# Optimization experiments

Hardware: AMD Instinct MI355X
Metric: run time of the kernel (lower is better)

Reference implementation:

```python
import jax, jax.numpy as jnp
import numpy as np

N_NODES = 50000
N_EDGES = 1000000
NUM_FEATURES = 32
EDGE_DIM = 16
H = 64
L = 2
BN_EPS = 1e-5
GIN_EPS = 0.0


def _lin(k, fan_in, fan_out, scale=0.1):
    kw, kb = jax.random.split(k)
    W = jax.random.normal(kw, (fan_in, fan_out), jnp.float32) * scale
    b = jax.random.normal(kb, (fan_out,), jnp.float32) * scale
    return W, b


def setup_inputs() -> dict:
    key = jax.random.key(0)
    ks = jax.random.split(key, 12)
    x = jax.random.normal(ks[0], (N_NODES, NUM_FEATURES), jnp.float32)
    edge_index = jax.random.randint(ks[1], (2, N_EDGES), 0, N_NODES, jnp.int64 if jax.config.read('jax_enable_x64') else jnp.int32)
    edge_attr = jax.random.normal(ks[2], (N_EDGES, EDGE_DIM), jnp.float32)
    node_W, node_b = _lin(ks[3], NUM_FEATURES, H)
    edge_W, edge_b = _lin(ks[4], EDGE_DIM, H)

    def stack_lin(k, fan_in, fan_out):
        Ws, bs = zip(*[_lin(kk, fan_in, fan_out) for kk in jax.random.split(k, L)])
        return jnp.stack(Ws), jnp.stack(bs)

    elin_W, elin_b = stack_lin(ks[5], H, H)      # GINEConv internal edge lin
    mlp1_W, mlp1_b = stack_lin(ks[6], H, H)      # GINEConv nn layer 1
    mlp2_W, mlp2_b = stack_lin(ks[7], H, H)      # GINEConv nn layer 2
    emlp1_W, emlp1_b = stack_lin(ks[8], 3 * H, H)  # edge-update MLP layer 1
    emlp2_W, emlp2_b = stack_lin(ks[9], H, H)      # edge-update MLP layer 2
    bn_gamma = jnp.ones((L, H), jnp.float32)
    bn_beta = jnp.zeros((L, H), jnp.float32)
    return dict(x=x, edge_index=edge_index, edge_attr=edge_attr,
                node_W=node_W, node_b=node_b, edge_W=edge_W, edge_b=edge_b,
                elin_W=elin_W, elin_b=elin_b,
                mlp1_W=mlp1_W, mlp1_b=mlp1_b, mlp2_W=mlp2_W, mlp2_b=mlp2_b,
                emlp1_W=emlp1_W, emlp1_b=emlp1_b, emlp2_W=emlp2_W, emlp2_b=emlp2_b,
                bn_gamma=bn_gamma, bn_beta=bn_beta)


def reference(x, edge_index, edge_attr,
              node_W, node_b, edge_W, edge_b,
              elin_W, elin_b, mlp1_W, mlp1_b, mlp2_W, mlp2_b,
              emlp1_W, emlp1_b, emlp2_W, emlp2_b, bn_gamma, bn_beta):
    src, dst = edge_index[0], edge_index[1]
    n = x.shape[0]
    h = x @ node_W + node_b                     # [N, H]
    ea = edge_attr @ edge_W + edge_b            # [E, H]
    for i in range(L):
        # GINEConv: message = relu(x_src + lin(edge_attr)), sum-aggregate at dst
        msg = jax.nn.relu(h[src] + ea @ elin_W[i] + elin_b[i])        # [E, H]
        agg = jax.ops.segment_sum(msg, dst, num_segments=n)           # [N, H]
        out = (1.0 + GIN_EPS) * h + agg
        out = jax.nn.relu(out @ mlp1_W[i] + mlp1_b[i]) @ mlp2_W[i] + mlp2_b[i]
        # BatchNorm (training-mode batch statistics, biased variance)
        mu = out.mean(axis=0)
        var = out.var(axis=0)
        out = (out - mu) * jax.lax.rsqrt(var + BN_EPS) * bn_gamma[i] + bn_beta[i]
        h = (h + jax.nn.relu(out)) * 0.5
        # edge update: gather-concat-MLP residual
        e_in = jnp.concatenate([h[src], h[dst], ea], axis=-1)         # [E, 3H]
        e_up = jax.nn.relu(e_in @ emlp1_W[i] + emlp1_b[i]) @ emlp2_W[i] + emlp2_b[i]
        ea = ea + e_up * 0.5
    return h, ea
```

## Files before the change

kernel.cpp:

```cpp
#include <hip/hip_runtime.h>
#include <hip/hip_bf16.h>

#define NN 50000
#define NE 1000000
#define NF 32
#define ED 16
#define HD 64
#define BN_EPS 1e-5f

typedef unsigned short u16;
typedef __attribute__((ext_vector_type(8))) short bf16x8;
typedef __attribute__((ext_vector_type(4))) float f32x4;

#define WAVE_SYNC() do { \
    asm volatile("s_waitcnt lgkmcnt(0)" ::: "memory"); \
    __builtin_amdgcn_sched_barrier(0); \
} while (0)

__device__ __forceinline__ u16 f2b(float x)
{
    __hip_bfloat16 b = __float2bfloat16(x);
    u16 u; __builtin_memcpy(&u, &b, 2); return u;
}
__device__ __forceinline__ float b2f(u16 u)
{
    uint v = (uint)u << 16; float f; __builtin_memcpy(&f, &v, 4); return f;
}

__global__ __launch_bounds__(256) void k_fill(float* p, float v, size_t n)
{
    size_t i = (size_t)blockIdx.x * 256 + threadIdx.x;
    if (i < n) p[i] = v;
}

__device__ __forceinline__ void gemm4(float (&o)[HD], float4 t, const float* __restrict__ Wr)
{
    #pragma unroll
    for (int f = 0; f < HD; f++) o[f] = fmaf(t.x, Wr[f], o[f]);
    #pragma unroll
    for (int f = 0; f < HD; f++) o[f] = fmaf(t.y, Wr[HD + f], o[f]);
    #pragma unroll
    for (int f = 0; f < HD; f++) o[f] = fmaf(t.z, Wr[2 * HD + f], o[f]);
    #pragma unroll
    for (int f = 0; f < HD; f++) o[f] = fmaf(t.w, Wr[3 * HD + f], o[f]);
}

__device__ __forceinline__ bf16x8 pack8(const float* __restrict__ p)
{
    float4 v0 = ((const float4*)p)[0];
    float4 v1 = ((const float4*)p)[1];
    union { uint u[4]; bf16x8 v; } r;
    r.u[0] = (uint)f2b(v0.x) | ((uint)f2b(v0.y) << 16);
    r.u[1] = (uint)f2b(v0.z) | ((uint)f2b(v0.w) << 16);
    r.u[2] = (uint)f2b(v1.x) | ((uint)f2b(v1.y) << 16);
    r.u[3] = (uint)f2b(v1.z) | ((uint)f2b(v1.w) << 16);
    return r.v;
}

__global__ __launch_bounds__(256) void k_prep_all(
    const float* __restrict__ W1, const float* __restrict__ W2,
    const float* __restrict__ We, const float* __restrict__ Wp,
    u16* __restrict__ w1t, u16* __restrict__ w2t,
    u16* __restrict__ welt, u16* __restrict__ wpad)
{
    int idx = blockIdx.x * 256 + threadIdx.x;
    if (idx < 24576) {
        int l = idx / (192 * HD), r = idx % (192 * HD), k = r / HD, f = r % HD;
        w1t[l * 192 * HD + f * 192 + k] = f2b(W1[idx]);
    } else if (idx < 32768) {
        int i = idx - 24576;
        int l = i / (HD * HD), r = i % (HD * HD), k = r / HD, f = r % HD;
        w2t[l * HD * HD + f * HD + k] = f2b(W2[i]);
    } else if (idx < 40960) {
        int i = idx - 32768;
        int l = i / (HD * HD), r = i % (HD * HD), k = r / HD, f = r % HD;
        welt[l * HD * HD + f * HD + k] = f2b(We[i]);
    } else if (idx < 43008) {
        int i = idx - 40960;
        int f = i / 32, k = i % 32;
        wpad[f * 32 + k] = (k < ED) ? f2b(Wp[k * HD + f]) : (u16)0;
    }
}

__global__ __launch_bounds__(256) void k_node_proj(
    const float* __restrict__ x, const float* __restrict__ W,
    const float* __restrict__ b, float* __restrict__ h, float* __restrict__ agg)
{
    __shared__ float sW[NF * HD];
    for (int t = threadIdx.x; t < NF * HD; t += 256) sW[t] = W[t];
    __syncthreads();
    int lane = threadIdx.x & 63, wv = threadIdx.x >> 6;
    int n = blockIdx.x * 4 + wv;
    if (n >= NN) return;
    float a = (lane < NF) ? x[(size_t)n * NF + lane] : 0.f;
    float acc = b[lane];
    #pragma unroll
    for (int k = 0; k < NF; k++) acc = fmaf(__shfl(a, k), sW[k * HD + lane], acc);
    h[(size_t)n * HD + lane] = acc;
    agg[(size_t)n * HD + lane] = 0.f;
}

__global__ __launch_bounds__(256) void k_edge_proj_gine(
    const float* __restrict__ attr, const float* __restrict__ h,
    const int* __restrict__ src, const int* __restrict__ dst,
    const u16* __restrict__ wpadt, const float* __restrict__ eb,
    const u16* __restrict__ welt, const float* __restrict__ belin,
    u16* __restrict__ eab, float* __restrict__ agg, float* __restrict__ bnst)
{
    __shared__ u16 sO[4][32 * 72];
    const int lane = threadIdx.x & 63, wv = threadIdx.x >> 6;
    if (blockIdx.x == 0 && threadIdx.x < 128) bnst[threadIdx.x] = 0.f;
    const size_t base = ((size_t)blockIdx.x * 4 + wv) * 32;
    if (base >= NE) return;
    u16* sOw = sO[wv];
    const int c = lane & 15, g = lane >> 4;

    bf16x8 zero8 = {0, 0, 0, 0, 0, 0, 0, 0};
    bf16x8 ap[2];
    #pragma unroll
    for (int s = 0; s < 2; s++)
        ap[s] = (g < 2) ? pack8(attr + (base + 16 * s + c) * ED + 8 * g) : zero8;

    f32x4 acc[2][4];
    #pragma unroll
    for (int s = 0; s < 2; s++)
        #pragma unroll
        for (int tt = 0; tt < 4; tt++) {
            float bv = eb[tt * 16 + c];
            acc[s][tt] = (f32x4){bv, bv, bv, bv};
        }
    #pragma unroll
    for (int tt = 0; tt < 4; tt++) {
        bf16x8 bw = *(const bf16x8*)&wpadt[(tt * 16 + c) * 32 + 8 * g];
        acc[0][tt] = __builtin_amdgcn_mfma_f32_16x16x32_bf16(ap[0], bw, acc[0][tt], 0, 0, 0);
        acc[1][tt] = __builtin_amdgcn_mfma_f32_16x16x32_bf16(ap[1], bw, acc[1][tt], 0, 0, 0);
    }
    #pragma unroll
    for (int s = 0; s < 2; s++)
        #pragma unroll
        for (int tt = 0; tt < 4; tt++)
            #pragma unroll
            for (int r = 0; r < 4; r++) {
                u16 nb = f2b(acc[s][tt][r]);
                eab[(base + 16 * s + 4 * g + r) * HD + tt * 16 + c] = nb;
                sOw[(16 * s + 4 * g + r) * 72 + tt * 16 + c] = nb;
            }
    WAVE_SYNC();

    bf16x8 A3[2][2];
    #pragma unroll
    for (int s = 0; s < 2; s++) {
        A3[s][0] = *(const bf16x8*)&sOw[(16 * s + c) * 72 + 8 * g];
        A3[s][1] = *(const bf16x8*)&sOw[(16 * s + c) * 72 + 32 + 8 * g];
    }
    f32x4 acc3[2][4];
    #pragma unroll
    for (int s = 0; s < 2; s++)
        #pragma unroll
        for (int tt = 0; tt < 4; tt++) {
            float bv = belin[tt * 16 + c];
            acc3[s][tt] = (f32x4){bv, bv, bv, bv};
        }
    #pragma unroll
    for (int ki = 0; ki < 2; ki++)
        #pragma unroll
        for (int tt = 0; tt < 4; tt++) {
            bf16x8 bw = *(const bf16x8*)&welt[(tt * 16 + c) * HD + ki * 32 + 8 * g];
            acc3[0][tt] = __builtin_amdgcn_mfma_f32_16x16x32_bf16(A3[0][ki], bw, acc3[0][tt], 0, 0, 0);
            acc3[1][tt] = __builtin_amdgcn_mfma_f32_16x16x32_bf16(A3[1][ki], bw, acc3[1][tt], 0, 0, 0);
        }
    int sv2[2][4], dv2[2][4];
    #pragma unroll
    for (int s = 0; s < 2; s++)
        #pragma unroll
        for (int r = 0; r < 4; r++) {
            sv2[s][r] = src[base + 16 * s + 4 * g + r];
            dv2[s][r] = dst[base + 16 * s + 4 * g + r];
        }
    #pragma unroll
    for (int s = 0; s < 2; s++)
        #pragma unroll
        for (int tt = 0; tt < 4; tt++)
            #pragma unroll
            for (int r = 0; r < 4; r++) {
                float m = fmaxf(acc3[s][tt][r] + h[(size_t)sv2[s][r] * HD + tt * 16 + c], 0.f);
                unsafeAtomicAdd(&agg[(size_t)dv2[s][r] * HD + tt * 16 + c], m);
            }
}

__global__ __launch_bounds__(256) void k_node_mlp(
    const float* __restrict__ h, const float* __restrict__ agg,
    const float* __restrict__ W1, const float* __restrict__ b1,
    const float* __restrict__ W2, const float* __restrict__ b2,
    float* __restrict__ out2)
{
    int n = blockIdx.x * 256 + threadIdx.x;
    if (n >= NN) return;
    float o[HD];
    #pragma unroll
    for (int f = 0; f < HD; f++) o[f] = b1[f];
    const float4* hr = (const float4*)(h + (size_t)n * HD);
    const float4* ar = (const float4*)(agg + (size_t)n * HD);
    #pragma unroll 4
    for (int k4 = 0; k4 < 16; k4++) {
        float4 t1 = hr[k4], t2 = ar[k4];
        float4 t = make_float4(t1.x + t2.x, t1.y + t2.y, t1.z + t2.z, t1.w + t2.w);
        gemm4(o, t, W1 + (k4 * 4) * HD);
    }
    #pragma unroll
    for (int k = 0; k < HD; k++) o[k] = fmaxf(o[k], 0.f);
    #pragma unroll
    for (int c = 0; c < 4; c++) {
        float p[16];
        #pragma unroll
        for (int j = 0; j < 16; j++) p[j] = b2[c * 16 + j];
        for (int k = 0; k < HD; k++) {
            const float* Wr = W2 + k * HD + c * 16;
            #pragma unroll
            for (int j = 0; j < 16; j++) p[j] = fmaf(o[k], Wr[j], p[j]);
        }
        float4* orow = (float4*)(out2 + (size_t)n * HD + c * 16);
        #pragma unroll
        for (int q = 0; q < 4; q++)
            orow[q] = make_float4(p[4*q], p[4*q+1], p[4*q+2], p[4*q+3]);
    }
}

__global__ __launch_bounds__(256) void k_bnstats(
    const float* __restrict__ out2, float* __restrict__ bnst)
{
    int f = threadIdx.x & 63;
    int row0 = blockIdx.x * 4 + (threadIdx.x >> 6);
    float s = 0.f, q = 0.f;
    for (int r = row0; r < NN; r += gridDim.x * 4) {
        float v = out2[(size_t)r * HD + f];
        s += v; q += v * v;
    }
    unsafeAtomicAdd(&bnst[f], s);
    unsafeAtomicAdd(&bnst[HD + f], q);
}

__global__ __launch_bounds__(256) void k_bn_h(
    const float* __restrict__ out2, const float* __restrict__ bnst,
    const float* __restrict__ gamma, const float* __restrict__ beta,
    float* __restrict__ h, u16* __restrict__ hbf, float* __restrict__ hout,
    float* __restrict__ agg, int last)
{
    size_t idx = (size_t)blockIdx.x * 256 + threadIdx.x;
    if (idx >= (size_t)NN * HD) return;
    int f = (int)(idx & 63);
    float mu  = bnst[f] * (1.f / NN);
    float var = bnst[HD + f] * (1.f / NN) - mu * mu;
    float sc  = gamma[f] * rsqrtf(var + BN_EPS);
    float sh  = beta[f] - mu * sc;
    float o   = fmaxf(fmaf(out2[idx], sc, sh), 0.f);
    float hn  = (h[idx] + o) * 0.5f;
    h[idx] = hn;
    hbf[idx] = f2b(hn);
    if (last) hout[idx] = hn;
    else      agg[idx] = 0.f;
}

__device__ __forceinline__ void edge_mlp_core(
    const u16* __restrict__ hbf, const u16* __restrict__ eab,
    const int* __restrict__ src, const int* __restrict__ dst,
    const u16* __restrict__ w1t, const float* __restrict__ b1,
    const u16* __restrict__ w2t, const float* __restrict__ b2,
    u16* sOw, size_t base, int c, int g, f32x4 (&acc2)[2][4])
{
    int sv[2], dv[2];
    #pragma unroll
    for (int s = 0; s < 2; s++) {
        sv[s] = src[base + 16 * s + c];
        dv[s] = dst[base + 16 * s + c];
    }
    bf16x8 A[3][2][2];
    #pragma unroll
    for (int s = 0; s < 2; s++) {
        const u16* hs = &hbf[(size_t)sv[s] * HD + 8 * g];
        A[0][s][0] = *(const bf16x8*)hs;
        A[0][s][1] = *(const bf16x8*)(hs + 32);
        const u16* hd = &hbf[(size_t)dv[s] * HD + 8 * g];
        A[1][s][0] = *(const bf16x8*)hd;
        A[1][s][1] = *(const bf16x8*)(hd + 32);
        const u16* ep = &eab[(base + 16 * s + c) * HD + 8 * g];
        A[2][s][0] = *(const bf16x8*)ep;
        A[2][s][1] = *(const bf16x8*)(ep + 32);
    }
    f32x4 acc[2][4];
    #pragma unroll
    for (int s = 0; s < 2; s++)
        #pragma unroll
        for (int tt = 0; tt < 4; tt++) {
            float bv = b1[tt * 16 + c];
            acc[s][tt] = (f32x4){bv, bv, bv, bv};
        }
    #pragma unroll
    for (int sec = 0; sec < 3; sec++)
        #pragma unroll
        for (int ki = 0; ki < 2; ki++)
            #pragma unroll
            for (int tt = 0; tt < 4; tt++) {
                bf16x8 bw = *(const bf16x8*)&w1t[(tt * 16 + c) * 192 + sec * 64 + ki * 32 + 8 * g];
                acc[0][tt] = __builtin_amdgcn_mfma_f32_16x16x32_bf16(A[sec][0][ki], bw, acc[0][tt], 0, 0, 0);
                acc[1][tt] = __builtin_amdgcn_mfma_f32_16x16x32_bf16(A[sec][1][ki], bw, acc[1][tt], 0, 0, 0);
            }
    #pragma unroll
    for (int s = 0; s < 2; s++)
        #pragma unroll
        for (int tt = 0; tt < 4; tt++)
            #pragma unroll
            for (int r = 0; r < 4; r++)
                sOw[(16 * s + 4 * g + r) * 72 + tt * 16 + c] = f2b(fmaxf(acc[s][tt][r], 0.f));
    WAVE_SYNC();
    bf16x8 A2[2][2];
    #pragma unroll
    for (int s = 0; s < 2; s++) {
        A2[s][0] = *(const bf16x8*)&sOw[(16 * s + c) * 72 + 8 * g];
        A2[s][1] = *(const bf16x8*)&sOw[(16 * s + c) * 72 + 32 + 8 * g];
    }
    WAVE_SYNC();
    #pragma unroll
    for (int s = 0; s < 2; s++)
        #pragma unroll
        for (int tt = 0; tt < 4; tt++) {
            float bv = b2[tt * 16 + c];
            acc2[s][tt] = (f32x4){bv, bv, bv, bv};
        }
    #pragma unroll
    for (int ki = 0; ki < 2; ki++)
        #pragma unroll
        for (int tt = 0; tt < 4; tt++) {
            bf16x8 bw = *(const bf16x8*)&w2t[(tt * 16 + c) * HD + ki * 32 + 8 * g];
            acc2[0][tt] = __builtin_amdgcn_mfma_f32_16x16x32_bf16(A2[0][ki], bw, acc2[0][tt], 0, 0, 0);
            acc2[1][tt] = __builtin_amdgcn_mfma_f32_16x16x32_bf16(A2[1][ki], bw, acc2[1][tt], 0, 0, 0);
        }
}

__global__ __launch_bounds__(256) void k_edge_upd_fused(
    const u16* __restrict__ hbf, u16* __restrict__ eab,
    const int* __restrict__ src, const int* __restrict__ dst,
    const u16* __restrict__ w1t, const float* __restrict__ b1,
    const u16* __restrict__ w2t, const float* __restrict__ b2,
    const float* __restrict__ h, const u16* __restrict__ welt,
    const float* __restrict__ belin, float* __restrict__ agg,
    float* __restrict__ bnst)
{
    __shared__ u16 sO[4][32 * 72];
    const int lane = threadIdx.x & 63, wv = threadIdx.x >> 6;
    if (blockIdx.x == 0 && threadIdx.x < 128) bnst[threadIdx.x] = 0.f;
    const size_t base = ((size_t)blockIdx.x * 4 + wv) * 32;
    if (base >= NE) return;
    u16* sOw = sO[wv];
    const int c = lane & 15, g = lane >> 4;

    f32x4 acc2[2][4];
    edge_mlp_core(hbf, eab, src, dst, w1t, b1, w2t, b2, sOw, base, c, g, acc2);

    #pragma unroll
    for (int s = 0; s < 2; s++)
        #pragma unroll
        for (int tt = 0; tt < 4; tt++)
            #pragma unroll
            for (int r = 0; r < 4; r++) {
                size_t a = (base + 16 * s + 4 * g + r) * HD + tt * 16 + c;
                u16 nb = f2b(b2f(eab[a]) + 0.5f * acc2[s][tt][r]);
                eab[a] = nb;
                sOw[(16 * s + 4 * g + r) * 72 + tt * 16 + c] = nb;
            }
    WAVE_SYNC();

    bf16x8 A3[2][2];
    #pragma unroll
    for (int s = 0; s < 2; s++) {
        A3[s][0] = *(const bf16x8*)&sOw[(16 * s + c) * 72 + 8 * g];
        A3[s][1] = *(const bf16x8*)&sOw[(16 * s + c) * 72 + 32 + 8 * g];
    }
    f32x4 acc3[2][4];
    #pragma unroll
    for (int s = 0; s < 2; s++)
        #pragma unroll
        for (int tt = 0; tt < 4; tt++) {
            float bv = belin[tt * 16 + c];
            acc3[s][tt] = (f32x4){bv, bv, bv, bv};
        }
    #pragma unroll
    for (int ki = 0; ki < 2; ki++)
        #pragma unroll
        for (int tt = 0; tt < 4; tt++) {
            bf16x8 bw = *(const bf16x8*)&welt[(tt * 16 + c) * HD + ki * 32 + 8 * g];
            acc3[0][tt] = __builtin_amdgcn_mfma_f32_16x16x32_bf16(A3[0][ki], bw, acc3[0][tt], 0, 0, 0);
            acc3[1][tt] = __builtin_amdgcn_mfma_f32_16x16x32_bf16(A3[1][ki], bw, acc3[1][tt], 0, 0, 0);
        }
    int sv2[2][4], dv2[2][4];
    #pragma unroll
    for (int s = 0; s < 2; s++)
        #pragma unroll
        for (int r = 0; r < 4; r++) {
            sv2[s][r] = src[base + 16 * s + 4 * g + r];
            dv2[s][r] = dst[base + 16 * s + 4 * g + r];
        }
    #pragma unroll
    for (int s = 0; s < 2; s++)
        #pragma unroll
        for (int tt = 0; tt < 4; tt++)
            #pragma unroll
            for (int r = 0; r < 4; r++) {
                float m = fmaxf(acc3[s][tt][r] + h[(size_t)sv2[s][r] * HD + tt * 16 + c], 0.f);
                unsafeAtomicAdd(&agg[(size_t)dv2[s][r] * HD + tt * 16 + c], m);
            }
}

__global__ __launch_bounds__(256) void k_edge_upd_final(
    const u16* __restrict__ hbf, const u16* __restrict__ eab,
    float* __restrict__ eaout,
    const int* __restrict__ src, const int* __restrict__ dst,
    const u16* __restrict__ w1t, const float* __restrict__ b1,
    const u16* __restrict__ w2t, const float* __restrict__ b2)
{
    __shared__ u16 sO[4][32 * 72];
    const int lane = threadIdx.x & 63, wv = threadIdx.x >> 6;
    const size_t base = ((size_t)blockIdx.x * 4 + wv) * 32;
    if (base >= NE) return;
    u16* sOw = sO[wv];
    const int c = lane & 15, g = lane >> 4;

    f32x4 acc2[2][4];
    edge_mlp_core(hbf, eab, src, dst, w1t, b1, w2t, b2, sOw, base, c, g, acc2);

    #pragma unroll
    for (int s = 0; s < 2; s++)
        #pragma unroll
        for (int tt = 0; tt < 4; tt++)
            #pragma unroll
            for (int r = 0; r < 4; r++) {
                size_t a = (base + 16 * s + 4 * g + r) * HD + tt * 16 + c;
                eaout[a] = b2f(eab[a]) + 0.5f * acc2[s][tt][r];
            }
}

extern "C" void kernel_launch(void* const* d_in, const int* in_sizes, int n_in,
                              void* d_out, int out_size, void* d_ws, size_t ws_size,
                              hipStream_t stream)
{
    const float* x        = (const float*)d_in[0];
    const int*   ei       = (const int*)d_in[1];
    const float* eattr    = (const float*)d_in[2];
    const float* node_W   = (const float*)d_in[3];
    const float* node_b   = (const float*)d_in[4];
    const float* edge_W   = (const float*)d_in[5];
    const float* edge_b   = (const float*)d_in[6];
    const float* elin_W   = (const float*)d_in[7];
    const float* elin_b   = (const float*)d_in[8];
    const float* mlp1_W   = (const float*)d_in[9];
    const float* mlp1_b   = (const float*)d_in[10];
    const float* mlp2_W   = (const float*)d_in[11];
    const float* mlp2_b   = (const float*)d_in[12];
    const float* emlp1_W  = (const float*)d_in[13];
    const float* emlp1_b  = (const float*)d_in[14];
    const float* emlp2_W  = (const float*)d_in[15];
    const float* emlp2_b  = (const float*)d_in[16];
    const float* bn_gamma = (const float*)d_in[17];
    const float* bn_beta  = (const float*)d_in[18];

    float* hout = (float*)d_out;
    float* eaout = hout + (size_t)NN * HD;

    const int* src = ei;
    const int* dst = ei + NE;

    float* hbuf = (float*)d_ws;
    float* agg  = hbuf + (size_t)NN * HD;
    float* out2 = agg + (size_t)NN * HD;
    float* bnst = out2 + (size_t)NN * HD;
    u16*   w1t  = (u16*)(bnst + 128);
    u16*   w2t  = w1t + 2 * 192 * HD;
    u16*   welt = w2t + 2 * HD * HD;
    u16*   wpad = welt + 2 * HD * HD;
    u16*   hbf  = wpad + HD * 32;
    u16*   eab  = hbf + (size_t)NN * HD;
    size_t base_need = ((size_t)NN * HD * 3 + 128) * sizeof(float)
                     + (2 * 192 * HD + 4 * HD * HD + HD * 32 + (size_t)NN * HD
                        + (size_t)NE * HD) * sizeof(u16);

    static const int exp_sizes[19] = {
        1600000, 2000000, 16000000, 2048, 64, 1024, 64,
        8192, 128, 8192, 128, 8192, 128, 24576, 128, 8192, 128, 128, 128};
    float sentinel = 0.f;
    if (n_in != 19) sentinel = 6000.f;
    else {
        for (int i = 0; i < 19; i++)
            if (in_sizes[i] != exp_sizes[i]) { sentinel = 2000.f + 32.f * i; break; }
    }
    if (sentinel == 0.f && ws_size < base_need) sentinel = 7000.f;
    if (sentinel != 0.f) {
        k_fill<<<dim3((unsigned)(((size_t)NN * HD + 255) / 256)), dim3(256), 0, stream>>>(
            hout, sentinel, (size_t)NN * HD);
        k_fill<<<dim3((unsigned)(((size_t)NE * HD + 255) / 256)), dim3(256), 0, stream>>>(
            eaout, 0.f, (size_t)NE * HD);
        return;
    }

    dim3 b256(256);
    const unsigned WG2 = (NE + 127) / 128;
    k_prep_all<<<dim3((43008 + 255) / 256), b256, 0, stream>>>(
        emlp1_W, emlp2_W, elin_W, edge_W, w1t, w2t, welt, wpad);
    k_node_proj<<<dim3((NN + 3) / 4), b256, 0, stream>>>(x, node_W, node_b, hbuf, agg);

    k_edge_proj_gine<<<dim3(WG2), b256, 0, stream>>>(
        eattr, hbuf, src, dst, wpad, edge_b, welt, elin_b, eab, agg, bnst);
    k_node_mlp<<<dim3((NN + 255) / 256), b256, 0, stream>>>(
        hbuf, agg, mlp1_W, mlp1_b, mlp2_W, mlp2_b, out2);
    k_bnstats<<<dim3(256), b256, 0, stream>>>(out2, bnst);
    k_bn_h<<<dim3((NN * HD + 255) / 256), b256, 0, stream>>>(
        out2, bnst, bn_gamma, bn_beta, hbuf, hbf, hout, agg, 0);
    k_edge_upd_fused<<<dim3(WG2), b256, 0, stream>>>(
        hbf, eab, src, dst, w1t, emlp1_b, w2t, emlp2_b,
        hbuf, welt + (size_t)HD * HD, elin_b + HD, agg, bnst);

    k_node_mlp<<<dim3((NN + 255) / 256), b256, 0, stream>>>(
        hbuf, agg, mlp1_W + HD * HD, mlp1_b + HD,
        mlp2_W + HD * HD, mlp2_b + HD, out2);
    k_bnstats<<<dim3(256), b256, 0, stream>>>(out2, bnst);
    k_bn_h<<<dim3((NN * HD + 255) / 256), b256, 0, stream>>>(
        out2, bnst, bn_gamma + HD, bn_beta + HD, hbuf, hbf, hout, agg, 1);
    k_edge_upd_final<<<dim3(WG2), b256, 0, stream>>>(
        hbf, eab, eaout, src, dst,
        w1t + (size_t)192 * HD, emlp1_b + HD,
        w2t + (size_t)HD * HD, emlp2_b + HD);
}
```

Baseline: 988.6 us.

## Replace atomic scatter-add aggregation with CSR gather over bf16 messages

Builds a destination-sorted CSR (histogram, single-block scan, atomic scatter of edge ids) each call. The GINE message kernels now write bf16 messages into the output buffer instead of doing float atomics into agg. A new per-node gather kernel then sums them. This removes 64M float atomics per layer and the agg zeroing, at the cost of CSR build kernels, an extra 128MB message write and read per layer, and bf16 rounding of messages before summation.

```diff
diff --git a/kernel.cpp b/kernel.cpp
--- a/kernel.cpp
+++ b/kernel.cpp
@@ -82,9 +82,68 @@
     }
 }
 
+__global__ __launch_bounds__(256) void k_hist(
+    const int* __restrict__ dst, int* __restrict__ cnt)
+{
+    for (size_t e = (size_t)blockIdx.x * 256 + threadIdx.x; e < NE;
+         e += (size_t)gridDim.x * 256)
+        atomicAdd(&cnt[dst[e]], 1);
+}
+#define SCHUNK 49
+__global__ __launch_bounds__(1024) void k_scan(
+    const int* __restrict__ cnt, int* __restrict__ rowptr, int* __restrict__ woff)
+{
+    __shared__ int ssum[1024];
+    int t = threadIdx.x;
+    int beg = t * SCHUNK, end = min(beg + SCHUNK, NN);
+    int s = 0;
+    for (int i = beg; i < end; i++) s += cnt[i];
+    ssum[t] = s;
+    __syncthreads();
+    for (int off = 1; off < 1024; off <<= 1) {
+        int v = (t >= off) ? ssum[t - off] : 0;
+        __syncthreads();
+        ssum[t] += v;
+        __syncthreads();
+    }
+    int run = (t == 0) ? 0 : ssum[t - 1];
+    for (int i = beg; i < end; i++) {
+        rowptr[i] = run; woff[i] = run;
+        run += cnt[i];
+    }
+    if (t == 1023) rowptr[NN] = run;
+}
+__global__ __launch_bounds__(256) void k_scatter(
+    const int* __restrict__ dst, int* __restrict__ woff, int* __restrict__ eidx)
+{
+    for (size_t e = (size_t)blockIdx.x * 256 + threadIdx.x; e < NE;
+         e += (size_t)gridDim.x * 256) {
+        int slot = atomicAdd(&woff[dst[e]], 1);
+        eidx[slot] = (int)e;
+    }
+}
+
+__global__ __launch_bounds__(256) void k_aggregate(
+    const u16* __restrict__ msg, const int* __restrict__ rowptr,
+    const int* __restrict__ eidx, float* __restrict__ agg)
+{
+    int lane = threadIdx.x & 63, wv = threadIdx.x >> 6;
+    int n = blockIdx.x * 4 + wv;
+    if (n >= NN) return;
+    int b = rowptr[n], e = rowptr[n + 1];
+    float s = 0.f;
+    int j = b;
+    for (; j + 1 < e; j += 2) {
+        int e0 = eidx[j], e1 = eidx[j + 1];
+        s += b2f(msg[(size_t)e0 * HD + lane]) + b2f(msg[(size_t)e1 * HD + lane]);
+    }
+    if (j < e) s += b2f(msg[(size_t)eidx[j] * HD + lane]);
+    agg[(size_t)n * HD + lane] = s;
+}
+
 __global__ __launch_bounds__(256) void k_node_proj(
     const float* __restrict__ x, const float* __restrict__ W,
-    const float* __restrict__ b, float* __restrict__ h, float* __restrict__ agg)
+    const float* __restrict__ b, float* __restrict__ h)
 {
     __shared__ float sW[NF * HD];
     for (int t = threadIdx.x; t < NF * HD; t += 256) sW[t] = W[t];
@@ -97,15 +156,14 @@
     #pragma unroll
     for (int k = 0; k < NF; k++) acc = fmaf(__shfl(a, k), sW[k * HD + lane], acc);
     h[(size_t)n * HD + lane] = acc;
-    agg[(size_t)n * HD + lane] = 0.f;
 }
 
 __global__ __launch_bounds__(256) void k_edge_proj_gine(
     const float* __restrict__ attr, const float* __restrict__ h,
-    const int* __restrict__ src, const int* __restrict__ dst,
+    const int* __restrict__ src,
     const u16* __restrict__ wpadt, const float* __restrict__ eb,
     const u16* __restrict__ welt, const float* __restrict__ belin,
-    u16* __restrict__ eab, float* __restrict__ agg, float* __restrict__ bnst)
+    u16* __restrict__ eab, u16* __restrict__ msgb, float* __restrict__ bnst)
 {
     __shared__ u16 sO[4][32 * 72];
     const int lane = threadIdx.x & 63, wv = threadIdx.x >> 6;
@@ -169,14 +227,12 @@
             acc3[0][tt] = __builtin_amdgcn_mfma_f32_16x16x32_bf16(A3[0][ki], bw, acc3[0][tt], 0, 0, 0);
             acc3[1][tt] = __builtin_amdgcn_mfma_f32_16x16x32_bf16(A3[1][ki], bw, acc3[1][tt], 0, 0, 0);
         }
-    int sv2[2][4], dv2[2][4];
-    #pragma unroll
-    for (int s = 0; s < 2; s++)
-        #pragma unroll
-        for (int r = 0; r < 4; r++) {
+    int sv2[2][4];
+    #pragma unroll
+    for (int s = 0; s < 2; s++)
+        #pragma unroll
+        for (int r = 0; r < 4; r++)
             sv2[s][r] = src[base + 16 * s + 4 * g + r];
-            dv2[s][r] = dst[base + 16 * s + 4 * g + r];
-        }
     #pragma unroll
     for (int s = 0; s < 2; s++)
         #pragma unroll
@@ -184,7 +240,7 @@
             #pragma unroll
             for (int r = 0; r < 4; r++) {
                 float m = fmaxf(acc3[s][tt][r] + h[(size_t)sv2[s][r] * HD + tt * 16 + c], 0.f);
-                unsafeAtomicAdd(&agg[(size_t)dv2[s][r] * HD + tt * 16 + c], m);
+                msgb[(base + 16 * s + 4 * g + r) * HD + tt * 16 + c] = f2b(m);
             }
 }
 
@@ -243,8 +299,7 @@
 __global__ __launch_bounds__(256) void k_bn_h(
     const float* __restrict__ out2, const float* __restrict__ bnst,
     const float* __restrict__ gamma, const float* __restrict__ beta,
-    float* __restrict__ h, u16* __restrict__ hbf, float* __restrict__ hout,
-    float* __restrict__ agg, int last)
+    float* __restrict__ h, u16* __restrict__ hbf, float* __restrict__ hout, int last)
 {
     size_t idx = (size_t)blockIdx.x * 256 + threadIdx.x;
     if (idx >= (size_t)NN * HD) return;
@@ -258,7 +313,6 @@
     h[idx] = hn;
     hbf[idx] = f2b(hn);
     if (last) hout[idx] = hn;
-    else      agg[idx] = 0.f;
 }
 
 __device__ __forceinline__ void edge_mlp_core(
@@ -343,7 +397,7 @@
     const u16* __restrict__ w1t, const float* __restrict__ b1,
     const u16* __restrict__ w2t, const float* __restrict__ b2,
     const float* __restrict__ h, const u16* __restrict__ welt,
-    const float* __restrict__ belin, float* __restrict__ agg,
+    const float* __restrict__ belin, u16* __restrict__ msgb,
     float* __restrict__ bnst)
 {
     __shared__ u16 sO[4][32 * 72];
@@ -392,14 +446,12 @@
             acc3[0][tt] = __builtin_amdgcn_mfma_f32_16x16x32_bf16(A3[0][ki], bw, acc3[0][tt], 0, 0, 0);
             acc3[1][tt] = __builtin_amdgcn_mfma_f32_16x16x32_bf16(A3[1][ki], bw, acc3[1][tt], 0, 0, 0);
         }
-    int sv2[2][4], dv2[2][4];
-    #pragma unroll
-    for (int s = 0; s < 2; s++)
-        #pragma unroll
-        for (int r = 0; r < 4; r++) {
+    int sv2[2][4];
+    #pragma unroll
+    for (int s = 0; s < 2; s++)
+        #pragma unroll
+        for (int r = 0; r < 4; r++)
             sv2[s][r] = src[base + 16 * s + 4 * g + r];
-            dv2[s][r] = dst[base + 16 * s + 4 * g + r];
-        }
     #pragma unroll
     for (int s = 0; s < 2; s++)
         #pragma unroll
@@ -407,7 +459,7 @@
             #pragma unroll
             for (int r = 0; r < 4; r++) {
                 float m = fmaxf(acc3[s][tt][r] + h[(size_t)sv2[s][r] * HD + tt * 16 + c], 0.f);
-                unsafeAtomicAdd(&agg[(size_t)dv2[s][r] * HD + tt * 16 + c], m);
+                msgb[(base + 16 * s + 4 * g + r) * HD + tt * 16 + c] = f2b(m);
             }
 }
 
@@ -465,6 +517,7 @@
 
     float* hout = (float*)d_out;
     float* eaout = hout + (size_t)NN * HD;
+    u16* msgb = (u16*)eaout;
 
     const int* src = ei;
     const int* dst = ei + NE;
@@ -473,13 +526,18 @@
     float* agg  = hbuf + (size_t)NN * HD;
     float* out2 = agg + (size_t)NN * HD;
     float* bnst = out2 + (size_t)NN * HD;
-    u16*   w1t  = (u16*)(bnst + 128);
+    int*   cnt    = (int*)(bnst + 128);
+    int*   rowptr = cnt + NN;
+    int*   woff   = rowptr + NN + 1;
+    int*   eidx   = woff + NN;
+    u16*   w1t  = (u16*)(eidx + NE);
     u16*   w2t  = w1t + 2 * 192 * HD;
     u16*   welt = w2t + 2 * HD * HD;
     u16*   wpad = welt + 2 * HD * HD;
     u16*   hbf  = wpad + HD * 32;
     u16*   eab  = hbf + (size_t)NN * HD;
     size_t base_need = ((size_t)NN * HD * 3 + 128) * sizeof(float)
+                     + ((size_t)3 * NN + 1 + NE) * sizeof(int)
                      + (2 * 192 * HD + 4 * HD * HD + HD * 32 + (size_t)NN * HD
                         + (size_t)NE * HD) * sizeof(u16);
 
@@ -503,27 +561,35 @@
 
     dim3 b256(256);
     const unsigned WG2 = (NE + 127) / 128;
+    const unsigned AGG_G = (NN + 3) / 4;
+
+    hipMemsetAsync(cnt, 0, NN * sizeof(int), stream);
     k_prep_all<<<dim3((43008 + 255) / 256), b256, 0, stream>>>(
         emlp1_W, emlp2_W, elin_W, edge_W, w1t, w2t, welt, wpad);
-    k_node_proj<<<dim3((NN + 3) / 4), b256, 0, stream>>>(x, node_W, node_b, hbuf, agg);
+    k_node_proj<<<dim3((NN + 3) / 4), b256, 0, stream>>>(x, node_W, node_b, hbuf);
+    k_hist<<<dim3(1024), b256, 0, stream>>>(dst, cnt);
+    k_scan<<<dim3(1), dim3(1024), 0, stream>>>(cnt, rowptr, woff);
+    k_scatter<<<dim3(1024), b256, 0, stream>>>(dst, woff, eidx);
 
     k_edge_proj_gine<<<dim3(WG2), b256, 0, stream>>>(
-        eattr, hbuf, src, dst, wpad, edge_b, welt, elin_b, eab, agg, bnst);
+        eattr, hbuf, src, wpad, edge_b, welt, elin_b, eab, msgb, bnst);
+    k_aggregate<<<dim3(AGG_G), b256, 0, stream>>>(msgb, rowptr, eidx, agg);
     k_node_mlp<<<dim3((NN + 255) / 256), b256, 0, stream>>>(
         hbuf, agg, mlp1_W, mlp1_b, mlp2_W, mlp2_b, out2);
     k_bnstats<<<dim3(256), b256, 0, stream>>>(out2, bnst);
     k_bn_h<<<dim3((NN * HD + 255) / 256), b256, 0, stream>>>(
-        out2, bnst, bn_gamma, bn_beta, hbuf, hbf, hout, agg, 0);
+        out2, bnst, bn_gamma, bn_beta, hbuf, hbf, hout, 0);
     k_edge_upd_fused<<<dim3(WG2), b256, 0, stream>>>(
         hbf, eab, src, dst, w1t, emlp1_b, w2t, emlp2_b,
-        hbuf, welt + (size_t)HD * HD, elin_b + HD, agg, bnst);
+        hbuf, welt + (size_t)HD * HD, elin_b + HD, msgb, bnst);
+    k_aggregate<<<dim3(AGG_G), b256, 0, stream>>>(msgb, rowptr, eidx, agg);
 
     k_node_mlp<<<dim3((NN + 255) / 256), b256, 0, stream>>>(
         hbuf, agg, mlp1_W + HD * HD, mlp1_b + HD,
         mlp2_W + HD * HD, mlp2_b + HD, out2);
     k_bnstats<<<dim3(256), b256, 0, stream>>>(out2, bnst);
     k_bn_h<<<dim3((NN * HD + 255) / 256), b256, 0, stream>>>(
-        out2, bnst, bn_gamma + HD, bn_beta + HD, hbuf, hbf, hout, agg, 1);
+        out2, bnst, bn_gamma + HD, bn_beta + HD, hbuf, hbf, hout, 1);
     k_edge_upd_final<<<dim3(WG2), b256, 0, stream>>>(
         hbf, eab, eaout, src, dst,
         w1t + (size_t)192 * HD, emlp1_b + HD,
```

New measurement: 1.308 ms. 32.3% more time.
